# Kernel tuning notes

Hardware: AMD Instinct MI355X
Metric: run time of the kernel (lower is better)

Reference implementation:

```python
import jax, jax.numpy as jnp
import numpy as np

D_MODEL = 256
SCALE = 1.0 / float(np.sqrt(D_MODEL))


def setup_inputs() -> dict:
    key = jax.random.key(0)
    kq, kk, kv, km = jax.random.split(key, 4)
    B, S, D = 16, 2048, D_MODEL
    q = jax.random.normal(kq, (B, S, D), dtype=jnp.float32)
    k = jax.random.normal(kk, (B, S, D), dtype=jnp.float32)
    v = jax.random.normal(kv, (B, S, D), dtype=jnp.float32)
    mask = jax.random.randint(km, (1, S, S), 0, 2, dtype=jnp.int32)
    return {"q": q, "k": k, "v": v, "mask": mask}


def reference(q, k, v, mask):
    # scores: [B, S, S] = q @ k^T * scale
    scores = jnp.einsum("bqd,bkd->bqk", q, k) * SCALE
    scores = jnp.where(mask == 0, -jnp.inf, scores)
    attn_weights = jax.nn.softmax(scores, axis=-1)
    output = jnp.einsum("bqk,bkd->bqd", attn_weights, v)
    return (output, attn_weights)
```

## Files before the change

### kernel.cpp

```cpp
#include <hip/hip_runtime.h>
#include <hip/hip_bf16.h>
#include <stdint.h>


#define B_ 16
#define S_ 2048
#define D_ 256
#define SCALE_ 0.0625f

typedef __attribute__((ext_vector_type(8))) short bf16x8;
typedef __attribute__((ext_vector_type(4))) float f32x4;

__device__ __forceinline__ uint16_t f2bf(float f) {
  uint32_t u = __float_as_uint(f);
  u += 0x7fffu + ((u >> 16) & 1u);
  return (uint16_t)(u >> 16);
}

typedef __attribute__((address_space(3))) uint32_t lds_u32;
typedef __attribute__((address_space(1))) const uint32_t glb_u32;
__device__ __forceinline__ void gload_lds16(const void* g, void* l) {
  __builtin_amdgcn_global_load_lds((glb_u32*)g, (lds_u32*)l, 16, 0, 0);
}

__global__ void k_convert(const float* __restrict__ src, uint16_t* __restrict__ dst) {
  const int t = blockIdx.x * blockDim.x + threadIdx.x;
  const float4* s = (const float4*)src + (size_t)t * 2;
  float4 a = s[0], b = s[1];
  ushort4 lo = { f2bf(a.x), f2bf(a.y), f2bf(a.z), f2bf(a.w) };
  ushort4 hi = { f2bf(b.x), f2bf(b.y), f2bf(b.z), f2bf(b.w) };
  ((ushort4*)dst)[(size_t)t * 2]     = lo;
  ((ushort4*)dst)[(size_t)t * 2 + 1] = hi;
}

__global__ void k_transpose(const float* __restrict__ V, uint16_t* __restrict__ Vt) {
  __shared__ float tile[64][68];
  const int b = blockIdx.z, kv0 = blockIdx.x * 64, d0 = blockIdx.y * 64;
  const int t = threadIdx.x;
  {
    const int r = t >> 2, c = (t & 3) * 16;
    const float4* src = (const float4*)(V + ((size_t)b * S_ + kv0 + r) * D_ + d0 + c);
    float4 x0 = src[0], x1 = src[1], x2 = src[2], x3 = src[3];
    *(float4*)&tile[r][c]      = x0;
    *(float4*)&tile[r][c + 4]  = x1;
    *(float4*)&tile[r][c + 8]  = x2;
    *(float4*)&tile[r][c + 12] = x3;
  }
  __syncthreads();
  {
    const int dl = t >> 2, c = (t & 3) * 16;
    uint16_t o[16];
#pragma unroll
    for (int i = 0; i < 16; ++i) o[i] = f2bf(tile[c + i][dl]);
    uint16_t* dst = Vt + ((size_t)b * D_ + d0 + dl) * S_ + kv0 + c;
#pragma unroll
    for (int i = 0; i < 4; ++i) {
      ushort4 v4 = { o[4*i], o[4*i+1], o[4*i+2], o[4*i+3] };
      *(ushort4*)(dst + 4*i) = v4;
    }
  }
}

__global__ void k_maskpack(const int* __restrict__ mask, unsigned long long* __restrict__ Mb) {
  const int wid  = blockIdx.x * 4 + (threadIdx.x >> 6);
  const int lane = threadIdx.x & 63;
  const int row = wid >> 5, w64 = wid & 31;
  const int m = mask[(size_t)row * S_ + w64 * 64 + lane];
  unsigned long long bits = __ballot(m != 0);
  if (lane == 0) Mb[row * 32 + w64] = bits;
}

__global__ __launch_bounds__(256, 2) void k_attn(
    const float* __restrict__ Q, const uint16_t* __restrict__ Kb,
    const unsigned long long* __restrict__ Mb,
    float* __restrict__ E, float* __restrict__ Winv) {
  __shared__ uint16_t Ks[2][64 * 256];
  const int bid = blockIdx.x;
  const int swz = (bid & 7) * 64 + (bid >> 3);
  const int b = swz >> 5, q0 = (swz & 31) * 64;
  const int tid = threadIdx.x, w = tid >> 6, lane = tid & 63;
  const int wq = w >> 1, wkv = w & 1;
  const int l15 = lane & 15, lq = lane >> 4;
  const int qbase = q0 + wq * 32;

  bf16x8 aq[2][8];
#pragma unroll
  for (int qt = 0; qt < 2; ++qt) {
    const float* qrow = Q + ((size_t)b * S_ + qbase + qt * 16 + l15) * D_;
#pragma unroll
    for (int dc = 0; dc < 8; ++dc) {
      const float4* p = (const float4*)(qrow + dc * 32 + lq * 8);
      float4 x = p[0], y = p[1];
      union { bf16x8 v; uint16_t u[8]; } fr;
      fr.u[0] = f2bf(x.x); fr.u[1] = f2bf(x.y); fr.u[2] = f2bf(x.z); fr.u[3] = f2bf(x.w);
      fr.u[4] = f2bf(y.x); fr.u[5] = f2bf(y.y); fr.u[6] = f2bf(y.z); fr.u[7] = f2bf(y.w);
      aq[qt][dc] = fr.v;
    }
  }

  float rowpart[2][4] = {{0.f,0.f,0.f,0.f},{0.f,0.f,0.f,0.f}};

  auto stage = [&](int t) {
    const uint16_t* tbase = Kb + ((size_t)b * S_ + t * 64) * D_;
    uint16_t* lbase = Ks[t & 1];
#pragma unroll
    for (int it = 0; it < 8; ++it) {
      const int s = (it * 4 + w) * 64 + lane;
      const int r = s >> 5, c = s & 31;
      const int g = (c & ~7) | ((c ^ r) & 7);
      gload_lds16(tbase + (size_t)r * D_ + g * 8, lbase + (size_t)(it * 4 + w) * 64 * 8);
    }
  };

  stage(0);

  for (int t = 0; t < 32; ++t) {
    __syncthreads();
    if (t + 1 < 32) stage(t + 1);
    const uint16_t* kbuf = Ks[t & 1];

    f32x4 acc[2][2];
#pragma unroll
    for (int qt = 0; qt < 2; ++qt)
#pragma unroll
      for (int kt = 0; kt < 2; ++kt) acc[qt][kt] = 0.f;

#pragma unroll
    for (int dc = 0; dc < 8; ++dc) {
      bf16x8 bk[2];
#pragma unroll
      for (int kt = 0; kt < 2; ++kt) {
        const int kvl = wkv * 32 + kt * 16 + l15;
        const int g = dc * 4 + lq;
        const int gs = (g & ~7) | ((g ^ kvl) & 7);
        bk[kt] = *(const bf16x8*)&kbuf[(kvl * 32 + gs) * 8];
      }
      __builtin_amdgcn_s_setprio(1);
#pragma unroll
      for (int qt = 0; qt < 2; ++qt)
#pragma unroll
        for (int kt = 0; kt < 2; ++kt)
          acc[qt][kt] = __builtin_amdgcn_mfma_f32_16x16x32_bf16(
              aq[qt][dc], bk[kt], acc[qt][kt], 0, 0, 0);
      __builtin_amdgcn_s_setprio(0);
    }

    const int kvb = t * 64;
#pragma unroll
    for (int qt = 0; qt < 2; ++qt) {
#pragma unroll
      for (int r = 0; r < 4; ++r) {
        const int row = qbase + qt * 16 + lq * 4 + r;
        const unsigned long long mw = Mb[(size_t)row * 32 + t];
        float* erow = E + (size_t)b * S_ * S_ + (size_t)row * S_ + kvb + wkv * 32 + l15;
#pragma unroll
        for (int kt = 0; kt < 2; ++kt) {
          const float sc = acc[qt][kt][r] * SCALE_;
          const int bit = wkv * 32 + kt * 16 + l15;
          const float e = ((mw >> bit) & 1ull) ? __expf(sc) : 0.0f;
          rowpart[qt][r] += e;
          erow[kt * 16] = e;
        }
      }
    }
  }

#pragma unroll
  for (int qt = 0; qt < 2; ++qt)
#pragma unroll
    for (int r = 0; r < 4; ++r) {
      float vs = rowpart[qt][r];
      vs += __shfl_xor(vs, 1); vs += __shfl_xor(vs, 2);
      vs += __shfl_xor(vs, 4); vs += __shfl_xor(vs, 8);
      rowpart[qt][r] = vs;
    }
  __syncthreads();
  float* red = (float*)(void*)Ks[0];
  if (l15 == 0) {
#pragma unroll
    for (int qt = 0; qt < 2; ++qt)
#pragma unroll
      for (int r = 0; r < 4; ++r)
        red[wkv * 64 + wq * 32 + qt * 16 + lq * 4 + r] = rowpart[qt][r];
  }
  __syncthreads();
  if (wkv == 0 && l15 == 0) {
#pragma unroll
    for (int qt = 0; qt < 2; ++qt)
#pragma unroll
      for (int r = 0; r < 4; ++r) {
        const int rl = wq * 32 + qt * 16 + lq * 4 + r;
        Winv[(size_t)b * S_ + q0 + rl] = 1.0f / (red[rl] + red[64 + rl]);
      }
  }
}

__global__ __launch_bounds__(512, 4) void k_out(
    float* __restrict__ attn, const uint16_t* __restrict__ Vt,
    const float* __restrict__ Winv, float* __restrict__ O) {
  __shared__ uint16_t As[2][64 * 64];
  __shared__ uint16_t Vs[2][256 * 64];
  const int bid = blockIdx.x;
  const int swz = (bid & 7) * 64 + (bid >> 3);
  const int b = swz >> 5, q0 = (swz & 31) * 64;
  const int tid = threadIdx.x, w = tid >> 6, lane = tid & 63;
  const int l15 = lane & 15, lq = lane >> 4;
  const int srow = tid >> 3;
  const int scol = (tid & 7) * 8;
  const float inv_r = Winv[(size_t)b * S_ + q0 + srow];
  float* aprow = attn + ((size_t)b * S_ + q0 + srow) * S_ + scol;

  f32x4 acc[4][2];
#pragma unroll
  for (int qt = 0; qt < 4; ++qt)
#pragma unroll
    for (int dt = 0; dt < 2; ++dt) acc[qt][dt] = 0.f;

  f32x4 e0, e1;

  auto stageV = [&](int t) {
    const uint16_t* tbase = Vt + (size_t)b * D_ * S_ + t * 64;
    uint16_t* lbase = Vs[t & 1];
#pragma unroll
    for (int it = 0; it < 4; ++it) {
      const int s = (it * 8 + w) * 64 + lane;
      const int d = s >> 3, c = s & 7;
      const int g = c ^ (d & 7);
      gload_lds16(tbase + (size_t)d * S_ + g * 8, lbase + (size_t)(it * 8 + w) * 64 * 8);
    }
  };
  auto loadE = [&](int t) {
    const f32x4* ap = (const f32x4*)(aprow + (size_t)t * 64);
    e0 = ap[0];
    e1 = ap[1];
  };
  auto procE = [&](int t) {
    e0 *= inv_r; e1 *= inv_r;
    f32x4* ap = (f32x4*)(aprow + (size_t)t * 64);
    ap[0] = e0;
    ap[1] = e1;
    union { uint4 u; uint16_t h[8]; } g0;
    g0.h[0] = f2bf(e0[0]); g0.h[1] = f2bf(e0[1]); g0.h[2] = f2bf(e0[2]); g0.h[3] = f2bf(e0[3]);
    g0.h[4] = f2bf(e1[0]); g0.h[5] = f2bf(e1[1]); g0.h[6] = f2bf(e1[2]); g0.h[7] = f2bf(e1[3]);
    const int gc = tid & 7;
    uint16_t* abuf = As[t & 1];
    *(uint4*)&abuf[(srow * 8 + (gc ^ (srow & 7))) * 8] = g0.u;
  };

  stageV(0);
  loadE(0);
  procE(0);

  for (int t = 0; t < 32; ++t) {
    __syncthreads();
    if (t + 1 < 32) { stageV(t + 1); loadE(t + 1); }
    const uint16_t* abuf = As[t & 1];
    const uint16_t* vbuf = Vs[t & 1];

#pragma unroll
    for (int kc = 0; kc < 2; ++kc) {
      bf16x8 af[4], bv[2];
      const int g = kc * 4 + lq;
#pragma unroll
      for (int qt = 0; qt < 4; ++qt) {
        const int ql = qt * 16 + l15;
        af[qt] = *(const bf16x8*)&abuf[(ql * 8 + (g ^ (ql & 7))) * 8];
      }
#pragma unroll
      for (int dt = 0; dt < 2; ++dt) {
        const int dl = w * 32 + dt * 16 + l15;
        bv[dt] = *(const bf16x8*)&vbuf[(dl * 8 + (g ^ (dl & 7))) * 8];
      }
      __builtin_amdgcn_s_setprio(1);
#pragma unroll
      for (int qt = 0; qt < 4; ++qt)
#pragma unroll
        for (int dt = 0; dt < 2; ++dt)
          acc[qt][dt] = __builtin_amdgcn_mfma_f32_16x16x32_bf16(af[qt], bv[dt], acc[qt][dt], 0, 0, 0);
      __builtin_amdgcn_s_setprio(0);
    }
    if (t + 1 < 32) procE(t + 1);
  }

#pragma unroll
  for (int qt = 0; qt < 4; ++qt)
#pragma unroll
    for (int dt = 0; dt < 2; ++dt)
#pragma unroll
      for (int r = 0; r < 4; ++r)
        O[((size_t)b * S_ + q0 + qt * 16 + lq * 4 + r) * D_ +
          w * 32 + dt * 16 + l15] = acc[qt][dt][r];
}

extern "C" void kernel_launch(void* const* d_in, const int* in_sizes, int n_in,
                              void* d_out, int out_size, void* d_ws, size_t ws_size,
                              hipStream_t stream) {
  const float* q = (const float*)d_in[0];
  const float* k = (const float*)d_in[1];
  const float* v = (const float*)d_in[2];
  const int* mask = (const int*)d_in[3];

  float* out  = (float*)d_out;
  float* attn = out + (size_t)B_ * S_ * D_;

  uint16_t* Kb = (uint16_t*)d_ws;
  uint16_t* Vt = Kb + (size_t)B_ * S_ * D_;
  unsigned long long* Mb = (unsigned long long*)(Vt + (size_t)B_ * S_ * D_);
  float* Winv = (float*)(Mb + (size_t)S_ * 32);

  k_convert<<<dim3(2048), dim3(512), 0, stream>>>(k, Kb);
  k_transpose<<<dim3(32, 4, 16), dim3(256), 0, stream>>>(v, Vt);
  k_maskpack<<<dim3(16384), dim3(256), 0, stream>>>(mask, Mb);
  k_attn<<<dim3(512), dim3(256), 0, stream>>>(q, Kb, Mb, attn, Winv);
  k_out<<<dim3(512), dim3(512), 0, stream>>>(attn, Vt, Winv, out);
}
```

Measured before the change: 569.5 us.

## Store unnormalized scores as bf16 in attn buffer and apply normalization late

k_attn now writes unnormalized exp scores as bf16 into the first half of each attn row, staged through LDS for coalesced 16-byte stores, instead of fp32 directly. k_out reads the bf16 values, writes normalized fp32 in place, and feeds the unnormalized bf16 straight to the MFMA, applying 1/rowsum to the output at the end. It iterates tiles in reverse so the fp32 writes never overwrite bf16 data not yet read. The aim is to halve intermediate traffic and drop a conversion, at the cost of bf16 rounding in the stored weights and extra LDS use in k_attn.

```diff
diff --git a/kernel.cpp b/kernel.cpp
--- a/kernel.cpp
+++ b/kernel.cpp
@@ -73,8 +73,9 @@
 __global__ __launch_bounds__(256, 2) void k_attn(
     const float* __restrict__ Q, const uint16_t* __restrict__ Kb,
     const unsigned long long* __restrict__ Mb,
-    float* __restrict__ E, float* __restrict__ Winv) {
+    uint16_t* __restrict__ Ebu, float* __restrict__ Winv) {
   __shared__ uint16_t Ks[2][64 * 256];
+  __shared__ uint16_t Et[2][64 * 64];
   const int bid = blockIdx.x;
   const int swz = (bid & 7) * 64 + (bid >> 3);
   const int b = swz >> 5, q0 = (swz & 31) * 64;
@@ -112,11 +113,24 @@
     }
   };
 
+  auto storeEt = [&](int t) {
+    const uint16_t* src = Et[t & 1];
+#pragma unroll
+    for (int i = 0; i < 2; ++i) {
+      const int c = i * 256 + tid;
+      const int row = c >> 3, cg = c & 7;
+      const bf16x8 vd = *(const bf16x8*)&src[row * 64 + cg * 8];
+      *(bf16x8*)&Ebu[((size_t)b * S_ + q0 + row) * (size_t)S_ * 2 +
+                     (size_t)t * 64 + cg * 8] = vd;
+    }
+  };
+
   stage(0);
 
   for (int t = 0; t < 32; ++t) {
     __syncthreads();
     if (t + 1 < 32) stage(t + 1);
+    if (t > 0) storeEt(t - 1);
     const uint16_t* kbuf = Ks[t & 1];
 
     f32x4 acc[2][2];
@@ -145,25 +159,28 @@
       __builtin_amdgcn_s_setprio(0);
     }
 
-    const int kvb = t * 64;
 #pragma unroll
     for (int qt = 0; qt < 2; ++qt) {
 #pragma unroll
       for (int r = 0; r < 4; ++r) {
-        const int row = qbase + qt * 16 + lq * 4 + r;
+        const int qloc = wq * 32 + qt * 16 + lq * 4 + r;
+        const int row = q0 + qloc;
         const unsigned long long mw = Mb[(size_t)row * 32 + t];
-        float* erow = E + (size_t)b * S_ * S_ + (size_t)row * S_ + kvb + wkv * 32 + l15;
 #pragma unroll
         for (int kt = 0; kt < 2; ++kt) {
           const float sc = acc[qt][kt][r] * SCALE_;
           const int bit = wkv * 32 + kt * 16 + l15;
-          const float e = ((mw >> bit) & 1ull) ? __expf(sc) : 0.0f;
-          rowpart[qt][r] += e;
-          erow[kt * 16] = e;
+          uint16_t eb = 0;
+          if ((mw >> bit) & 1ull) eb = f2bf(__expf(sc));
+          rowpart[qt][r] += __uint_as_float((uint32_t)eb << 16);
+          Et[t & 1][qloc * 64 + wkv * 32 + kt * 16 + l15] = eb;
         }
       }
     }
   }
+
+  __syncthreads();
+  storeEt(31);
 
 #pragma unroll
   for (int qt = 0; qt < 2; ++qt)
@@ -174,7 +191,6 @@
       vs += __shfl_xor(vs, 4); vs += __shfl_xor(vs, 8);
       rowpart[qt][r] = vs;
     }
-  __syncthreads();
   float* red = (float*)(void*)Ks[0];
   if (l15 == 0) {
 #pragma unroll
@@ -206,9 +222,11 @@
   const int tid = threadIdx.x, w = tid >> 6, lane = tid & 63;
   const int l15 = lane & 15, lq = lane >> 4;
   const int srow = tid >> 3;
-  const int scol = (tid & 7) * 8;
+  const int sc8 = (tid & 7) * 8;
   const float inv_r = Winv[(size_t)b * S_ + q0 + srow];
-  float* aprow = attn + ((size_t)b * S_ + q0 + srow) * S_ + scol;
+  const uint16_t* ebrow = (const uint16_t*)attn +
+      ((size_t)b * S_ + q0 + srow) * (size_t)S_ * 2 + sc8;
+  float* aprow = attn + ((size_t)b * S_ + q0 + srow) * S_ + sc8;
 
   f32x4 acc[4][2];
 #pragma unroll
@@ -216,7 +234,7 @@
 #pragma unroll
     for (int dt = 0; dt < 2; ++dt) acc[qt][dt] = 0.f;
 
-  f32x4 e0, e1;
+  union { uint4 u; uint16_t h[8]; } eu;
 
   auto stageV = [&](int t) {
     const uint16_t* tbase = Vt + (size_t)b * D_ * S_ + t * 64;
@@ -230,30 +248,29 @@
     }
   };
   auto loadE = [&](int t) {
-    const f32x4* ap = (const f32x4*)(aprow + (size_t)t * 64);
-    e0 = ap[0];
-    e1 = ap[1];
+    eu.u = *(const uint4*)(ebrow + (size_t)t * 64);
   };
   auto procE = [&](int t) {
-    e0 *= inv_r; e1 *= inv_r;
+    f32x4 a0, a1;
+#pragma unroll
+    for (int j = 0; j < 4; ++j) {
+      a0[j] = __uint_as_float((uint32_t)eu.h[j] << 16) * inv_r;
+      a1[j] = __uint_as_float((uint32_t)eu.h[4 + j] << 16) * inv_r;
+    }
     f32x4* ap = (f32x4*)(aprow + (size_t)t * 64);
-    ap[0] = e0;
-    ap[1] = e1;
-    union { uint4 u; uint16_t h[8]; } g0;
-    g0.h[0] = f2bf(e0[0]); g0.h[1] = f2bf(e0[1]); g0.h[2] = f2bf(e0[2]); g0.h[3] = f2bf(e0[3]);
-    g0.h[4] = f2bf(e1[0]); g0.h[5] = f2bf(e1[1]); g0.h[6] = f2bf(e1[2]); g0.h[7] = f2bf(e1[3]);
+    ap[0] = a0;
+    ap[1] = a1;
     const int gc = tid & 7;
-    uint16_t* abuf = As[t & 1];
-    *(uint4*)&abuf[(srow * 8 + (gc ^ (srow & 7))) * 8] = g0.u;
-  };
-
-  stageV(0);
-  loadE(0);
-  procE(0);
-
-  for (int t = 0; t < 32; ++t) {
+    *(uint4*)&As[t & 1][(srow * 8 + (gc ^ (srow & 7))) * 8] = eu.u;
+  };
+
+  stageV(31);
+  loadE(31);
+  procE(31);
+
+  for (int t = 31; t >= 0; --t) {
     __syncthreads();
-    if (t + 1 < 32) { stageV(t + 1); loadE(t + 1); }
+    if (t > 0) { stageV(t - 1); loadE(t - 1); }
     const uint16_t* abuf = As[t & 1];
     const uint16_t* vbuf = Vs[t & 1];
 
@@ -279,17 +296,19 @@
           acc[qt][dt] = __builtin_amdgcn_mfma_f32_16x16x32_bf16(af[qt], bv[dt], acc[qt][dt], 0, 0, 0);
       __builtin_amdgcn_s_setprio(0);
     }
-    if (t + 1 < 32) procE(t + 1);
+    if (t > 0) procE(t - 1);
   }
 
 #pragma unroll
   for (int qt = 0; qt < 4; ++qt)
 #pragma unroll
-    for (int dt = 0; dt < 2; ++dt)
-#pragma unroll
-      for (int r = 0; r < 4; ++r)
+    for (int r = 0; r < 4; ++r) {
+      const float invq = Winv[(size_t)b * S_ + q0 + qt * 16 + lq * 4 + r];
+#pragma unroll
+      for (int dt = 0; dt < 2; ++dt)
         O[((size_t)b * S_ + q0 + qt * 16 + lq * 4 + r) * D_ +
-          w * 32 + dt * 16 + l15] = acc[qt][dt][r];
+          w * 32 + dt * 16 + l15] = acc[qt][dt][r] * invq;
+    }
 }
 
 extern "C" void kernel_launch(void* const* d_in, const int* in_sizes, int n_in,
@@ -311,6 +330,6 @@
   k_convert<<<dim3(2048), dim3(512), 0, stream>>>(k, Kb);
   k_transpose<<<dim3(32, 4, 16), dim3(256), 0, stream>>>(v, Vt);
   k_maskpack<<<dim3(16384), dim3(256), 0, stream>>>(mask, Mb);
-  k_attn<<<dim3(512), dim3(256), 0, stream>>>(q, Kb, Mb, attn, Winv);
+  k_attn<<<dim3(512), dim3(256), 0, stream>>>(q, Kb, Mb, (uint16_t*)attn, Winv);
   k_out<<<dim3(512), dim3(512), 0, stream>>>(attn, Vt, Winv, out);
 }
```

New measurement: 567.0 us. No clear change (-0.4%).
